# Kernel tuning notes

Measured on AMD Instinct MI355X. Metric: run time of the kernel, lower is better.

The kernel has to match this reference:

```python
import jax, jax.numpy as jnp
import numpy as np

N_NODES = 50000
NEG_SLOPE = 0.2
EPS = 1e-16


def add_self_loops(edge_index, n):
    loops = jnp.arange(n, dtype=edge_index.dtype)
    src = jnp.concatenate([edge_index[0], loops])
    dst = jnp.concatenate([edge_index[1], loops])
    return src, dst


def gatv2_conv(x, src, dst, Wl, Wr, att, b, heads, out_ch, concat):
    n = x.shape[0]
    # x_l: transformed source-side features (messages); x_r: target-side
    x_l = (x @ Wl).reshape(n, heads, out_ch)
    x_r = (x @ Wr).reshape(n, heads, out_ch)
    # per-edge GATv2 attention logits: a^T leaky_relu(xl_j + xr_i)
    e = jax.nn.leaky_relu(x_l[src] + x_r[dst], NEG_SLOPE)  # [E,H,D]
    logits = jnp.einsum('ehd,hd->eh', e, att.reshape(heads, out_ch))  # [E,H]
    # segment softmax over incoming edges per target node
    m = jax.ops.segment_max(logits, dst, num_segments=n)  # [N,H]
    m = jnp.where(jnp.isfinite(m), m, 0.0)
    ex = jnp.exp(logits - m[dst])
    denom = jax.ops.segment_sum(ex, dst, num_segments=n)  # [N,H]
    alpha = ex / (denom[dst] + EPS)  # [E,H]
    out = jax.ops.segment_sum(alpha[..., None] * x_l[src], dst, num_segments=n)  # [N,H,D]
    if concat:
        out = out.reshape(n, heads * out_ch)
    else:
        out = out.mean(axis=1)
    return out + b


def setup_inputs() -> dict:
    key = jax.random.key(0)
    ks = jax.random.split(key, 12)
    n, din, dh, heads, dout = N_NODES, 512, 16, 8, 64
    e = 800000
    x = jax.random.normal(ks[0], (n, din), dtype=jnp.float32)
    edge_index = jax.random.randint(ks[1], (2, e), 0, n, dtype=jnp.int32)
    s1 = 1.0 / np.sqrt(din)
    s2 = 1.0 / np.sqrt(dh * heads)
    return {
        'x': x,
        'edge_index': edge_index,
        'Wl1': jax.random.normal(ks[2], (din, dh * heads), dtype=jnp.float32) * s1,
        'Wr1': jax.random.normal(ks[3], (din, dh * heads), dtype=jnp.float32) * s1,
        'att1': jax.random.normal(ks[4], (heads, dh), dtype=jnp.float32) * s1,
        'b1': jax.random.normal(ks[5], (dh * heads,), dtype=jnp.float32) * 0.01,
        'Wl2': jax.random.normal(ks[6], (dh * heads, dout), dtype=jnp.float32) * s2,
        'Wr2': jax.random.normal(ks[7], (dh * heads, dout), dtype=jnp.float32) * s2,
        'att2': jax.random.normal(ks[8], (dout,), dtype=jnp.float32) * s2,
        'b2': jax.random.normal(ks[9], (dout,), dtype=jnp.float32) * 0.01,
    }


def reference(x, edge_index, Wl1, Wr1, att1, b1, Wl2, Wr2, att2, b2):
    n = x.shape[0]
    src, dst = add_self_loops(edge_index, n)
    # dropout is identity at inference
    h = gatv2_conv(x, src, dst, Wl1, Wr1, att1, b1, heads=8, out_ch=16, concat=True)
    h = jax.nn.elu(h)
    h = gatv2_conv(h, src, dst, Wl2, Wr2, att2, b2, heads=1, out_ch=64, concat=True)
    return jax.nn.log_softmax(h, axis=1)
```

## Files before the change

### kernel.cpp

```cpp
#include <hip/hip_runtime.h>
#include <math.h>

#define CDIV(a,b) (((a)+(b)-1)/(b))

typedef __bf16 bf16x8 __attribute__((ext_vector_type(8)));
typedef float  f32x4  __attribute__((ext_vector_type(4)));
typedef __attribute__((address_space(3))) uint32_t lds_u32_t;
typedef __attribute__((address_space(1))) uint32_t glb_u32_t;

__device__ __forceinline__ float lrelu(float v){ return v > 0.f ? v : 0.2f*v; }

__global__ void k_count_deg(const int* __restrict__ edst, int E, int ET, int* __restrict__ off){
  int e = blockIdx.x*blockDim.x + threadIdx.x;
  if (e >= ET) return;
  int d = (e < E) ? edst[e] : (e - E);
  atomicAdd(&off[d+1], 1);
}

__global__ __launch_bounds__(256) void k_scan_a(int* __restrict__ cnt, int n, int* __restrict__ bsum){
  int i = blockIdx.x*256 + threadIdx.x;
  int lane = threadIdx.x & 63, wv = threadIdx.x >> 6;
  int x = (i < n) ? cnt[i] : 0;
  #pragma unroll
  for (int d=1; d<64; d<<=1){ int y = __shfl_up(x, d, 64); if (lane >= d) x += y; }
  __shared__ int wsum[4];
  if (lane == 63) wsum[wv] = x;
  __syncthreads();
  #pragma unroll
  for (int j=0;j<3;j++) if (wv > j) x += wsum[j];
  if (i < n) cnt[i] = x;
  if (threadIdx.x == 255) bsum[blockIdx.x] = x;
}

__global__ __launch_bounds__(256) void k_scan_b(int* __restrict__ bsum, int nb){
  int t = threadIdx.x;
  int lane = t & 63, wv = t >> 6;
  int v = (t < nb) ? bsum[t] : 0;
  int x = v;
  #pragma unroll
  for (int d=1; d<64; d<<=1){ int y = __shfl_up(x, d, 64); if (lane >= d) x += y; }
  __shared__ int wsum[4];
  if (lane == 63) wsum[wv] = x;
  __syncthreads();
  #pragma unroll
  for (int j=0;j<3;j++) if (wv > j) x += wsum[j];
  if (t < nb) bsum[t] = x - v;
}

__global__ __launch_bounds__(256) void k_scan_c(int* __restrict__ off, int* __restrict__ cursor,
                                                const int* __restrict__ bsum, int n){
  int i = blockIdx.x*256 + threadIdx.x;
  if (i >= n) return;
  int v = off[1+i] + bsum[blockIdx.x];
  off[1+i] = v;
  if (i+1 < n) cursor[i+1] = v;
  if (i == 0) cursor[0] = 0;
}

__global__ void k_fill(const int* __restrict__ edst, int E, int ET,
                       int* __restrict__ cursor, int* __restrict__ adj){
  int e = blockIdx.x*blockDim.x + threadIdx.x;
  if (e >= ET) return;
  int d = (e < E) ? edst[e] : (e - E);
  int pos = atomicAdd(&cursor[d], 1);
  adj[pos] = e;
}

__global__ void k_cvt_bf16(const float* __restrict__ in, __bf16* __restrict__ out, int n4){
  int i = blockIdx.x*blockDim.x + threadIdx.x;
  if (i >= n4) return;
  float4 v = reinterpret_cast<const float4*>(in)[i];
  __bf16 o[4] = {(__bf16)v.x,(__bf16)v.y,(__bf16)v.z,(__bf16)v.w};
  *reinterpret_cast<ushort4*>(out + (size_t)i*4) =
      *reinterpret_cast<ushort4*>(o);
}

__global__ void k_prep_wt(const float* __restrict__ Wl, const float* __restrict__ Wr,
                          __bf16* __restrict__ Wt, int K, int Nh){
  int c = blockIdx.x, k = threadIdx.x;
  float v = (c < Nh) ? Wl[(size_t)k*Nh + c] : Wr[(size_t)k*Nh + (c - Nh)];
  Wt[(size_t)c*K + k] = (__bf16)v;
}

__global__ __launch_bounds__(256) void gemm_mfma(
    const __bf16* __restrict__ A, int M, int K,
    const __bf16* __restrict__ Bt, int N,
    __bf16* __restrict__ C)
{
  __shared__ __bf16 As[2][128*32];
  __shared__ __bf16 Bs[2][128*32];
  int tid = threadIdx.x;
  int w = tid >> 6, lane = tid & 63;
  int g = lane >> 4, r16 = lane & 15;
  int wr = w >> 1, wc = w & 1;
  int row0 = blockIdx.x * 128;
  int col0 = blockIdx.y * 128;
  int srow = tid >> 2, sslot = tid & 3;

  auto f = [](int r){ return (r + (r >> 2)) & 3; };

  f32x4 acc[4][4];
  #pragma unroll
  for (int m=0;m<4;m++)
    #pragma unroll
    for (int n=0;n<4;n++) acc[m][n] = (f32x4){0.f,0.f,0.f,0.f};

  auto STAGE = [&](int buf, int kt){
    #pragma unroll
    for (int i=0;i<2;i++){
      int trow = i*64 + srow;
      int arow = row0 + trow; if (arow >= M) arow = M-1;
      const __bf16* ga = A + (size_t)arow*K + kt*32 + ((sslot ^ f(trow))<<3);
      __builtin_amdgcn_global_load_lds((const glb_u32_t*)(const void*)ga,
          (lds_u32_t*)(void*)&As[buf][(i*64 + w*16)*32], 16, 0, 0);
      const __bf16* gb = Bt + (size_t)(col0 + trow)*K + kt*32 + ((sslot ^ f(trow))<<3);
      __builtin_amdgcn_global_load_lds((const glb_u32_t*)(const void*)gb,
          (lds_u32_t*)(void*)&Bs[buf][(i*64 + w*16)*32], 16, 0, 0);
    }
  };

  int nk = K >> 5;
  STAGE(0, 0);
  for (int kt = 0; kt < nk; ++kt){
    int cur = kt & 1;
    __syncthreads();
    if (kt+1 < nk) STAGE(cur^1, kt+1);
    bf16x8 a[4], b[4];
    #pragma unroll
    for (int m=0;m<4;m++){
      int row = wr*64 + m*16 + r16;
      a[m] = *reinterpret_cast<const bf16x8*>(&As[cur][row*32 + ((g ^ f(row))<<3)]);
    }
    #pragma unroll
    for (int n=0;n<4;n++){
      int row = wc*64 + n*16 + r16;
      b[n] = *reinterpret_cast<const bf16x8*>(&Bs[cur][row*32 + ((g ^ f(row))<<3)]);
    }
    #pragma unroll
    for (int m=0;m<4;m++)
      #pragma unroll
      for (int n=0;n<4;n++)
        acc[m][n] = __builtin_amdgcn_mfma_f32_16x16x32_bf16(a[m], b[n], acc[m][n], 0, 0, 0);
  }

  #pragma unroll
  for (int m=0;m<4;m++){
    int row_c = row0 + wr*64 + m*16 + g*4;
    #pragma unroll
    for (int n=0;n<4;n++){
      int col_c = col0 + wc*64 + n*16 + r16;
      #pragma unroll
      for (int r=0;r<4;r++)
        if (row_c + r < M) C[(size_t)(row_c+r)*N + col_c] = (__bf16)acc[m][n][r];
    }
  }
}

__global__ __launch_bounds__(128) void k_fused1(
    const int* __restrict__ off, const int* __restrict__ adj,
    const int* __restrict__ esrc, int E,
    const __bf16* __restrict__ H1, const float* __restrict__ att1,
    const float* __restrict__ b1, __bf16* __restrict__ out1)
{
  __shared__ __bf16 xls[16][132];
  __shared__ float  lgs[8][17];
  __shared__ float  ws [8][17];
  int i = blockIdx.x;
  int tid = threadIdx.x;
  int e_id = tid >> 3, h1 = tid & 7;
  int h2 = tid >> 4, d  = tid & 15;
  int begin = off[i], deg = off[i+1] - begin;

  float xr1[16], aw1[16];
  #pragma unroll
  for (int j=0;j<16;j++){
    xr1[j] = (float)H1[(size_t)i*256 + 128 + h1*16 + j];
    aw1[j] = att1[h1*16 + j];
  }

  float m_run = -INFINITY, s_run = 0.f, acc = 0.f;
  int nch = (deg + 15) >> 4;
  for (int ch=0; ch<nch; ch++){
    int base = ch*16;
    int cnt = min(16, deg - base);
    int k = base + e_id;
    if (e_id < cnt){
      int e = adj[begin + k];
      int s = (e < E) ? esrc[e] : (e - E);
      const __bf16* row = H1 + (size_t)s*256 + h1*16;
      bf16x8 v0 = *reinterpret_cast<const bf16x8*>(row);
      bf16x8 v1 = *reinterpret_cast<const bf16x8*>(row + 8);
      float lg = 0.f;
      #pragma unroll
      for (int j=0;j<8;j++){
        lg = fmaf(aw1[j],   lrelu((float)v0[j] + xr1[j]),   lg);
        lg = fmaf(aw1[j+8], lrelu((float)v1[j] + xr1[j+8]), lg);
      }
      lgs[h1][e_id] = lg;
      ushort4* dst = reinterpret_cast<ushort4*>(&xls[e_id][h1*16]);
      dst[0] = *reinterpret_cast<ushort4*>(&v0);
      dst[1] = *(reinterpret_cast<ushort4*>(&v0)+1);
      dst[2] = *reinterpret_cast<ushort4*>(&v1);
      dst[3] = *(reinterpret_cast<ushort4*>(&v1)+1);
    }
    __syncthreads();
    float m_c = -INFINITY;
    for (int j=0;j<cnt;j++) m_c = fmaxf(m_c, lgs[h2][j]);
    float m_new = fmaxf(m_run, m_c);
    float c = __expf(m_run - m_new);
    m_run = m_new;
    if (d < cnt) ws[h2][d] = __expf(lgs[h2][d] - m_new);
    __syncthreads();
    float s_c = 0.f, a_c = 0.f;
    for (int j=0;j<cnt;j++){
      float w = ws[h2][j];
      s_c += w;
      a_c = fmaf(w, (float)xls[j][h2*16 + d], a_c);
    }
    s_run = s_run*c + s_c;
    acc   = acc*c + a_c;
    __syncthreads();
  }
  float o = acc/(s_run + 1e-16f) + b1[tid];
  out1[(size_t)i*128 + tid] = (__bf16)(o > 0.f ? o : expm1f(o));
}

__global__ __launch_bounds__(64) void k_fused2(
    const int* __restrict__ off, const int* __restrict__ adj,
    const int* __restrict__ esrc, int E,
    const __bf16* __restrict__ H2, const float* __restrict__ att2,
    const float* __restrict__ b2, float* __restrict__ out)
{
  __shared__ __bf16 xls[64][68];
  __shared__ float  ws[64];
  __shared__ float  xr_s[64], aw_s[64];
  int i = blockIdx.x, lane = threadIdx.x;
  int begin = off[i], deg = off[i+1] - begin;
  xr_s[lane] = (float)H2[(size_t)i*128 + 64 + lane];
  aw_s[lane] = att2[lane];
  __syncthreads();

  float m_run = -INFINITY, s_run = 0.f, acc = 0.f;
  int nch = (deg + 63) >> 6;
  for (int ch=0; ch<nch; ch++){
    int base = ch*64;
    int cnt = min(64, deg - base);
    float lg = -INFINITY;
    if (lane < cnt){
      int e = adj[begin + base + lane];
      int s = (e < E) ? esrc[e] : (e - E);
      const __bf16* row = H2 + (size_t)s*128;
      float accl = 0.f;
      #pragma unroll
      for (int q=0;q<8;q++){
        bf16x8 v = *reinterpret_cast<const bf16x8*>(row + q*8);
        reinterpret_cast<ushort4*>(&xls[lane][0])[2*q]   = *reinterpret_cast<ushort4*>(&v);
        reinterpret_cast<ushort4*>(&xls[lane][0])[2*q+1] = *(reinterpret_cast<ushort4*>(&v)+1);
        #pragma unroll
        for (int j=0;j<8;j++)
          accl = fmaf(aw_s[q*8+j], lrelu((float)v[j] + xr_s[q*8+j]), accl);
      }
      lg = accl;
    }
    float m_c = lg;
    #pragma unroll
    for (int mm=1;mm<64;mm<<=1) m_c = fmaxf(m_c, __shfl_xor(m_c, mm, 64));
    float m_new = fmaxf(m_run, m_c);
    float c = __expf(m_run - m_new);
    float w = (lane < cnt) ? __expf(lg - m_new) : 0.f;
    float s_c = w;
    #pragma unroll
    for (int mm=1;mm<64;mm<<=1) s_c += __shfl_xor(s_c, mm, 64);
    ws[lane] = w;
    m_run = m_new;
    __syncthreads();
    float a_c = 0.f;
    for (int j=0;j<cnt;j++)
      a_c = fmaf(ws[j], (float)xls[j][lane], a_c);
    s_run = s_run*c + s_c;
    acc   = acc*c + a_c;
    __syncthreads();
  }
  float o = acc/(s_run + 1e-16f) + b2[lane];
  float mx = o;
  #pragma unroll
  for (int mm=1;mm<64;mm<<=1) mx = fmaxf(mx, __shfl_xor(mx,mm,64));
  float se = __expf(o - mx);
  #pragma unroll
  for (int mm=1;mm<64;mm<<=1) se += __shfl_xor(se,mm,64);
  out[(size_t)i*64 + lane] = o - mx - __logf(se);
}

extern "C" void kernel_launch(void* const* d_in, const int* in_sizes, int n_in,
                              void* d_out, int out_size, void* d_ws, size_t ws_size,
                              hipStream_t stream)
{
  const float* x    = (const float*)d_in[0];
  const int*   ei   = (const int*)  d_in[1];
  const float* Wl1  = (const float*)d_in[2];
  const float* Wr1  = (const float*)d_in[3];
  const float* att1 = (const float*)d_in[4];
  const float* b1   = (const float*)d_in[5];
  const float* Wl2  = (const float*)d_in[6];
  const float* Wr2  = (const float*)d_in[7];
  const float* att2 = (const float*)d_in[8];
  const float* b2   = (const float*)d_in[9];
  float* out = (float*)d_out;

  const int DIN = 512;
  int N  = in_sizes[0] / DIN;
  int E  = in_sizes[1] / 2;
  int ET = E + N;
  const int* esrc = ei;
  const int* edst = ei + E;

  char* p = (char*)d_ws;
  auto walloc = [&](size_t bytes)->void*{
    void* r = (void*)p; p += (bytes + 255) & ~(size_t)255; return r;
  };
  __bf16* xb   = (__bf16*)walloc((size_t)N*DIN*2);
  __bf16* Wt1  = (__bf16*)walloc((size_t)256*512*2);
  __bf16* Wt2  = (__bf16*)walloc((size_t)128*128*2);
  __bf16* H1   = (__bf16*)walloc((size_t)N*256*2);
  __bf16* out1 = (__bf16*)walloc((size_t)N*128*2);
  __bf16* H2   = (__bf16*)walloc((size_t)N*128*2);
  int* off    = (int*)walloc((size_t)(N+1)*4);
  int* cursor = (int*)walloc((size_t)N*4);
  int* adj    = (int*)walloc((size_t)ET*4);
  int* bsum   = (int*)walloc((size_t)256*4);

  int NB = CDIV(N,256);
  hipMemsetAsync(off, 0, (size_t)(N+1)*4, stream);
  k_count_deg<<<CDIV(ET,256),256,0,stream>>>(edst, E, ET, off);
  k_scan_a<<<NB,256,0,stream>>>(off+1, N, bsum);
  k_scan_b<<<1,256,0,stream>>>(bsum, NB);
  k_scan_c<<<NB,256,0,stream>>>(off, cursor, bsum, N);
  k_fill<<<CDIV(ET,256),256,0,stream>>>(edst, E, ET, cursor, adj);

  int n4 = N*DIN/4;
  k_cvt_bf16<<<CDIV(n4,256),256,0,stream>>>(x, xb, n4);
  k_prep_wt<<<256,512,0,stream>>>(Wl1, Wr1, Wt1, 512, 128);
  k_prep_wt<<<128,128,0,stream>>>(Wl2, Wr2, Wt2, 128, 64);

  dim3 g1(CDIV(N,128), 2);
  gemm_mfma<<<g1,256,0,stream>>>(xb, N, 512, Wt1, 256, H1);
  k_fused1<<<N,128,0,stream>>>(off, adj, esrc, E, H1, att1, b1, out1);

  dim3 g2(CDIV(N,128), 1);
  gemm_mfma<<<g2,256,0,stream>>>(out1, N, 128, Wt2, 128, H2);
  k_fused2<<<N,64,0,stream>>>(off, adj, esrc, E, H2, att2, b2, out);
}
```

Measured before the change: 487.5 us.

## Process one node per wavefront with per-lane online softmax in GAT aggregation

Both fused attention/aggregation kernels now assign one node per 64-lane wavefront and pack four nodes into each 256-thread block, replacing one block per node. Each lane keeps its own slice of edges, runs an online softmax with shuffle-based max reductions and accumulates features in registers. Partial sums are merged across lanes with shuffles at the end. This removes the LDS staging and the repeated __syncthreads per edge chunk, at the cost of a larger cross-lane reduction and more registers per lane. Leaky ReLU is also rewritten as a fmax.

```diff
diff --git a/kernel.cpp b/kernel.cpp
--- a/kernel.cpp
+++ b/kernel.cpp
@@ -8,7 +8,7 @@
 typedef __attribute__((address_space(3))) uint32_t lds_u32_t;
 typedef __attribute__((address_space(1))) uint32_t glb_u32_t;
 
-__device__ __forceinline__ float lrelu(float v){ return v > 0.f ? v : 0.2f*v; }
+__device__ __forceinline__ float lrelu(float v){ return fmaxf(v, 0.2f*v); }
 
 __global__ void k_count_deg(const int* __restrict__ edst, int E, int ET, int* __restrict__ off){
   int e = blockIdx.x*blockDim.x + threadIdx.x;
@@ -156,139 +156,182 @@
   }
 }
 
-__global__ __launch_bounds__(128) void k_fused1(
+__global__ __launch_bounds__(256) void k_fused1(
     const int* __restrict__ off, const int* __restrict__ adj,
-    const int* __restrict__ esrc, int E,
+    const int* __restrict__ esrc, int E, int N,
     const __bf16* __restrict__ H1, const float* __restrict__ att1,
     const float* __restrict__ b1, __bf16* __restrict__ out1)
 {
-  __shared__ __bf16 xls[16][132];
-  __shared__ float  lgs[8][17];
-  __shared__ float  ws [8][17];
-  int i = blockIdx.x;
-  int tid = threadIdx.x;
-  int e_id = tid >> 3, h1 = tid & 7;
-  int h2 = tid >> 4, d  = tid & 15;
-  int begin = off[i], deg = off[i+1] - begin;
-
-  float xr1[16], aw1[16];
-  #pragma unroll
-  for (int j=0;j<16;j++){
-    xr1[j] = (float)H1[(size_t)i*256 + 128 + h1*16 + j];
-    aw1[j] = att1[h1*16 + j];
-  }
-
-  float m_run = -INFINITY, s_run = 0.f, acc = 0.f;
-  int nch = (deg + 15) >> 4;
+  __shared__ float obuf[4][128];
+  int wid = threadIdx.x >> 6;
+  int node = blockIdx.x*4 + wid;
+  int nn = min(node, N-1);
+  int lane = threadIdx.x & 63;
+  int h = lane >> 3, e = lane & 7;
+  int begin = off[nn], deg = off[nn+1] - begin;
+
+  float xrf[16], aw[16];
+  {
+    const __bf16* xp = H1 + (size_t)nn*256 + 128 + h*16;
+    bf16x8 r0 = *reinterpret_cast<const bf16x8*>(xp);
+    bf16x8 r1 = *reinterpret_cast<const bf16x8*>(xp + 8);
+    #pragma unroll
+    for (int j=0;j<8;j++){ xrf[j] = (float)r0[j]; xrf[8+j] = (float)r1[j]; }
+    #pragma unroll
+    for (int q=0;q<4;q++){
+      float4 a4 = reinterpret_cast<const float4*>(att1 + h*16)[q];
+      aw[q*4+0]=a4.x; aw[q*4+1]=a4.y; aw[q*4+2]=a4.z; aw[q*4+3]=a4.w;
+    }
+  }
+
+  f32x4 acc[4];
+  #pragma unroll
+  for (int q=0;q<4;q++) acc[q] = (f32x4){0.f,0.f,0.f,0.f};
+  float s_p = 0.f, m_run = -INFINITY;
+
+  int nch = (deg + 7) >> 3;
   for (int ch=0; ch<nch; ch++){
-    int base = ch*16;
-    int cnt = min(16, deg - base);
-    int k = base + e_id;
-    if (e_id < cnt){
-      int e = adj[begin + k];
-      int s = (e < E) ? esrc[e] : (e - E);
-      const __bf16* row = H1 + (size_t)s*256 + h1*16;
-      bf16x8 v0 = *reinterpret_cast<const bf16x8*>(row);
-      bf16x8 v1 = *reinterpret_cast<const bf16x8*>(row + 8);
-      float lg = 0.f;
-      #pragma unroll
-      for (int j=0;j<8;j++){
-        lg = fmaf(aw1[j],   lrelu((float)v0[j] + xr1[j]),   lg);
-        lg = fmaf(aw1[j+8], lrelu((float)v1[j] + xr1[j+8]), lg);
-      }
-      lgs[h1][e_id] = lg;
-      ushort4* dst = reinterpret_cast<ushort4*>(&xls[e_id][h1*16]);
-      dst[0] = *reinterpret_cast<ushort4*>(&v0);
-      dst[1] = *(reinterpret_cast<ushort4*>(&v0)+1);
-      dst[2] = *reinterpret_cast<ushort4*>(&v1);
-      dst[3] = *(reinterpret_cast<ushort4*>(&v1)+1);
-    }
-    __syncthreads();
-    float m_c = -INFINITY;
-    for (int j=0;j<cnt;j++) m_c = fmaxf(m_c, lgs[h2][j]);
-    float m_new = fmaxf(m_run, m_c);
-    float c = __expf(m_run - m_new);
-    m_run = m_new;
-    if (d < cnt) ws[h2][d] = __expf(lgs[h2][d] - m_new);
-    __syncthreads();
-    float s_c = 0.f, a_c = 0.f;
-    for (int j=0;j<cnt;j++){
-      float w = ws[h2][j];
-      s_c += w;
-      a_c = fmaf(w, (float)xls[j][h2*16 + d], a_c);
-    }
-    s_run = s_run*c + s_c;
-    acc   = acc*c + a_c;
-    __syncthreads();
-  }
-  float o = acc/(s_run + 1e-16f) + b1[tid];
-  out1[(size_t)i*128 + tid] = (__bf16)(o > 0.f ? o : expm1f(o));
-}
-
-__global__ __launch_bounds__(64) void k_fused2(
+    int k = ch*8 + e;
+    int kc = min(k, deg-1);
+    int eidx = adj[begin + kc];
+    int s = (eidx < E) ? esrc[eidx] : (eidx - E);
+    const __bf16* xp = H1 + (size_t)s*256 + h*16;
+    bf16x8 v0 = *reinterpret_cast<const bf16x8*>(xp);
+    bf16x8 v1 = *reinterpret_cast<const bf16x8*>(xp + 8);
+    float xlf[16];
+    #pragma unroll
+    for (int j=0;j<8;j++){ xlf[j] = (float)v0[j]; xlf[8+j] = (float)v1[j]; }
+    float p = 0.f;
+    #pragma unroll
+    for (int j=0;j<16;j++) p = fmaf(aw[j], lrelu(xlf[j] + xrf[j]), p);
+    if (k >= deg) p = -INFINITY;
+    float mc = p;
+    mc = fmaxf(mc, __shfl_xor(mc,1,64));
+    mc = fmaxf(mc, __shfl_xor(mc,2,64));
+    mc = fmaxf(mc, __shfl_xor(mc,4,64));
+    float mnew = fmaxf(m_run, mc);
+    float c = __expf(m_run - mnew);
+    float w = (k < deg) ? __expf(p - mnew) : 0.f;
+    m_run = mnew;
+    s_p = s_p*c + w;
+    #pragma unroll
+    for (int j=0;j<16;j++) acc[j>>2][j&3] = fmaf(w, xlf[j], acc[j>>2][j&3]*c);
+  }
+  #pragma unroll
+  for (int mm=1;mm<8;mm<<=1){
+    #pragma unroll
+    for (int j=0;j<16;j++){
+      float t = __shfl_xor(acc[j>>2][j&3], mm, 64);
+      acc[j>>2][j&3] += t;
+    }
+    s_p += __shfl_xor(s_p, mm, 64);
+  }
+  if (e == 0){
+    #pragma unroll
+    for (int q=0;q<4;q++)
+      *reinterpret_cast<f32x4*>(&obuf[wid][h*16 + q*4]) = acc[q];
+  }
+  float inv = 1.f/(s_p + 1e-16f);
+  float2 ob = *reinterpret_cast<const float2*>(&obuf[wid][lane*2]);
+  float2 bb = *reinterpret_cast<const float2*>(b1 + lane*2);
+  float o0 = ob.x*inv + bb.x;
+  float o1 = ob.y*inv + bb.y;
+  o0 = o0 > 0.f ? o0 : expm1f(o0);
+  o1 = o1 > 0.f ? o1 : expm1f(o1);
+  union { __bf16 h2[2]; uint u; } pk;
+  pk.h2[0] = (__bf16)o0; pk.h2[1] = (__bf16)o1;
+  if (node < N)
+    *reinterpret_cast<uint*>(out1 + (size_t)node*128 + lane*2) = pk.u;
+}
+
+__global__ __launch_bounds__(256) void k_fused2(
     const int* __restrict__ off, const int* __restrict__ adj,
-    const int* __restrict__ esrc, int E,
+    const int* __restrict__ esrc, int E, int N,
     const __bf16* __restrict__ H2, const float* __restrict__ att2,
     const float* __restrict__ b2, float* __restrict__ out)
 {
-  __shared__ __bf16 xls[64][68];
-  __shared__ float  ws[64];
-  __shared__ float  xr_s[64], aw_s[64];
-  int i = blockIdx.x, lane = threadIdx.x;
-  int begin = off[i], deg = off[i+1] - begin;
-  xr_s[lane] = (float)H2[(size_t)i*128 + 64 + lane];
-  aw_s[lane] = att2[lane];
-  __syncthreads();
-
-  float m_run = -INFINITY, s_run = 0.f, acc = 0.f;
-  int nch = (deg + 63) >> 6;
+  __shared__ float obuf[4][64];
+  int wid = threadIdx.x >> 6;
+  int node = blockIdx.x*4 + wid;
+  int nn = min(node, N-1);
+  int lane = threadIdx.x & 63;
+  int q = lane >> 4, e = lane & 15;
+  int begin = off[nn], deg = off[nn+1] - begin;
+
+  float xrf[16], aw[16];
+  {
+    const __bf16* xp = H2 + (size_t)nn*128 + 64 + q*16;
+    bf16x8 r0 = *reinterpret_cast<const bf16x8*>(xp);
+    bf16x8 r1 = *reinterpret_cast<const bf16x8*>(xp + 8);
+    #pragma unroll
+    for (int j=0;j<8;j++){ xrf[j] = (float)r0[j]; xrf[8+j] = (float)r1[j]; }
+    #pragma unroll
+    for (int p4=0;p4<4;p4++){
+      float4 a4 = reinterpret_cast<const float4*>(att2 + q*16)[p4];
+      aw[p4*4+0]=a4.x; aw[p4*4+1]=a4.y; aw[p4*4+2]=a4.z; aw[p4*4+3]=a4.w;
+    }
+  }
+
+  f32x4 acc[4];
+  #pragma unroll
+  for (int p4=0;p4<4;p4++) acc[p4] = (f32x4){0.f,0.f,0.f,0.f};
+  float s_p = 0.f, m_run = -INFINITY;
+
+  int nch = (deg + 15) >> 4;
   for (int ch=0; ch<nch; ch++){
-    int base = ch*64;
-    int cnt = min(64, deg - base);
-    float lg = -INFINITY;
-    if (lane < cnt){
-      int e = adj[begin + base + lane];
-      int s = (e < E) ? esrc[e] : (e - E);
-      const __bf16* row = H2 + (size_t)s*128;
-      float accl = 0.f;
-      #pragma unroll
-      for (int q=0;q<8;q++){
-        bf16x8 v = *reinterpret_cast<const bf16x8*>(row + q*8);
-        reinterpret_cast<ushort4*>(&xls[lane][0])[2*q]   = *reinterpret_cast<ushort4*>(&v);
-        reinterpret_cast<ushort4*>(&xls[lane][0])[2*q+1] = *(reinterpret_cast<ushort4*>(&v)+1);
-        #pragma unroll
-        for (int j=0;j<8;j++)
-          accl = fmaf(aw_s[q*8+j], lrelu((float)v[j] + xr_s[q*8+j]), accl);
-      }
-      lg = accl;
-    }
-    float m_c = lg;
-    #pragma unroll
-    for (int mm=1;mm<64;mm<<=1) m_c = fmaxf(m_c, __shfl_xor(m_c, mm, 64));
-    float m_new = fmaxf(m_run, m_c);
-    float c = __expf(m_run - m_new);
-    float w = (lane < cnt) ? __expf(lg - m_new) : 0.f;
-    float s_c = w;
-    #pragma unroll
-    for (int mm=1;mm<64;mm<<=1) s_c += __shfl_xor(s_c, mm, 64);
-    ws[lane] = w;
-    m_run = m_new;
-    __syncthreads();
-    float a_c = 0.f;
-    for (int j=0;j<cnt;j++)
-      a_c = fmaf(ws[j], (float)xls[j][lane], a_c);
-    s_run = s_run*c + s_c;
-    acc   = acc*c + a_c;
-    __syncthreads();
-  }
-  float o = acc/(s_run + 1e-16f) + b2[lane];
+    int k = ch*16 + e;
+    int kc = min(k, deg-1);
+    int eidx = adj[begin + kc];
+    int s = (eidx < E) ? esrc[eidx] : (eidx - E);
+    const __bf16* xp = H2 + (size_t)s*128 + q*16;
+    bf16x8 v0 = *reinterpret_cast<const bf16x8*>(xp);
+    bf16x8 v1 = *reinterpret_cast<const bf16x8*>(xp + 8);
+    float xlf[16];
+    #pragma unroll
+    for (int j=0;j<8;j++){ xlf[j] = (float)v0[j]; xlf[8+j] = (float)v1[j]; }
+    float p = 0.f;
+    #pragma unroll
+    for (int j=0;j<16;j++) p = fmaf(aw[j], lrelu(xlf[j] + xrf[j]), p);
+    p += __shfl_xor(p,16,64);
+    p += __shfl_xor(p,32,64);
+    if (k >= deg) p = -INFINITY;
+    float mc = p;
+    mc = fmaxf(mc, __shfl_xor(mc,1,64));
+    mc = fmaxf(mc, __shfl_xor(mc,2,64));
+    mc = fmaxf(mc, __shfl_xor(mc,4,64));
+    mc = fmaxf(mc, __shfl_xor(mc,8,64));
+    float mnew = fmaxf(m_run, mc);
+    float c = __expf(m_run - mnew);
+    float w = (k < deg) ? __expf(p - mnew) : 0.f;
+    m_run = mnew;
+    s_p = s_p*c + w;
+    #pragma unroll
+    for (int j=0;j<16;j++) acc[j>>2][j&3] = fmaf(w, xlf[j], acc[j>>2][j&3]*c);
+  }
+  #pragma unroll
+  for (int mm=1;mm<16;mm<<=1){
+    #pragma unroll
+    for (int j=0;j<16;j++){
+      float t = __shfl_xor(acc[j>>2][j&3], mm, 64);
+      acc[j>>2][j&3] += t;
+    }
+    s_p += __shfl_xor(s_p, mm, 64);
+  }
+  if (e == 0){
+    #pragma unroll
+    for (int p4=0;p4<4;p4++)
+      *reinterpret_cast<f32x4*>(&obuf[wid][q*16 + p4*4]) = acc[p4];
+  }
+  float inv = 1.f/(s_p + 1e-16f);
+  float o = obuf[wid][lane]*inv + b2[lane];
   float mx = o;
   #pragma unroll
   for (int mm=1;mm<64;mm<<=1) mx = fmaxf(mx, __shfl_xor(mx,mm,64));
   float se = __expf(o - mx);
   #pragma unroll
   for (int mm=1;mm<64;mm<<=1) se += __shfl_xor(se,mm,64);
-  out[(size_t)i*64 + lane] = o - mx - __logf(se);
+  if (node < N)
+    out[(size_t)node*64 + lane] = o - mx - __logf(se);
 }
 
 extern "C" void kernel_launch(void* const* d_in, const int* in_sizes, int n_in,
@@ -344,9 +387,9 @@
 
   dim3 g1(CDIV(N,128), 2);
   gemm_mfma<<<g1,256,0,stream>>>(xb, N, 512, Wt1, 256, H1);
-  k_fused1<<<N,128,0,stream>>>(off, adj, esrc, E, H1, att1, b1, out1);
+  k_fused1<<<CDIV(N,4),256,0,stream>>>(off, adj, esrc, E, N, H1, att1, b1, out1);
 
   dim3 g2(CDIV(N,128), 1);
   gemm_mfma<<<g2,256,0,stream>>>(out1, N, 128, Wt2, 128, H2);
-  k_fused2<<<N,64,0,stream>>>(off, adj, esrc, E, H2, att2, b2, out);
-}
+  k_fused2<<<CDIV(N,4),256,0,stream>>>(off, adj, esrc, E, N, H2, att2, b2, out);
+}
```

After: 476.4 us. -2.3%, faster.
